# Kernel tuning notes

Measured on AMD Instinct MI355X. Metric: run time of the kernel, lower is better.

Reference implementation:

```python
import jax, jax.numpy as jnp
import numpy as np


def _conv_bn_relu(x, w, b, stride):
    # Conv2d(k=3, pad=1) with eval-mode BatchNorm folded into (w, b) at setup, then ReLU.
    y = jax.lax.conv_general_dilated(x, w, (stride, stride), ((1, 1), (1, 1)),
                                     dimension_numbers=('NCHW', 'OIHW', 'NCHW'))
    return jax.nn.relu(y + b[None, :, None, None])


def _affine_grid(theta, H, W):
    # torch.nn.functional.affine_grid, align_corners=False
    xs = (2.0 * jnp.arange(W, dtype=theta.dtype) + 1.0) / W - 1.0  # [W]
    ys = (2.0 * jnp.arange(H, dtype=theta.dtype) + 1.0) / H - 1.0  # [H]
    gx = theta[:, 0, 0, None, None] * xs[None, None, :] + theta[:, 0, 1, None, None] * ys[None, :, None] + theta[:, 0, 2, None, None]
    gy = theta[:, 1, 0, None, None] * xs[None, None, :] + theta[:, 1, 1, None, None] * ys[None, :, None] + theta[:, 1, 2, None, None]
    return jnp.stack([gx, gy], axis=-1)  # [B,H,W,2]


def _grid_sample_bilinear_zeros(im, grid):
    # torch.nn.functional.grid_sample, mode='bilinear', padding_mode='zeros', align_corners=False
    B, C, H, W = im.shape
    ix = ((grid[..., 0] + 1.0) * W - 1.0) * 0.5  # [B,H,W] pixel x coords
    iy = ((grid[..., 1] + 1.0) * H - 1.0) * 0.5
    x0 = jnp.floor(ix); y0 = jnp.floor(iy)
    x1 = x0 + 1.0;      y1 = y0 + 1.0
    wx1 = ix - x0; wx0 = 1.0 - wx1
    wy1 = iy - y0; wy0 = 1.0 - wy1
    imt = jnp.transpose(im, (0, 2, 3, 1))  # BHWC for channel-last gather
    bidx = jnp.arange(B)[:, None, None]

    def gather(xf, yf):
        valid = ((xf >= 0) & (xf <= W - 1) & (yf >= 0) & (yf <= H - 1)).astype(im.dtype)
        xi = jnp.clip(xf.astype(jnp.int32), 0, W - 1)
        yi = jnp.clip(yf.astype(jnp.int32), 0, H - 1)
        return imt[bidx, yi, xi] * valid[..., None]  # [B,H,W,C]

    out = (gather(x0, y0) * (wx0 * wy0)[..., None]
           + gather(x1, y0) * (wx1 * wy0)[..., None]
           + gather(x0, y1) * (wx0 * wy1)[..., None]
           + gather(x1, y1) * (wx1 * wy1)[..., None])
    return jnp.transpose(out, (0, 3, 1, 2))  # back to NCHW


def _forward(im_tensor, w1, b1, w2, b2, w3, b3, w4, b4, w5, b5, w6, b6,
             fw1, fb1, fw2, fb2, fw3, fb3):
    B, _, H, W = im_tensor.shape
    x1 = _conv_bn_relu(im_tensor, w1, b1, 1)
    x2 = _conv_bn_relu(jnp.concatenate([x1, im_tensor], 1), w2, b2, 2)
    x3 = _conv_bn_relu(x2, w3, b3, 1)
    x4 = _conv_bn_relu(jnp.concatenate([x3, x2], 1), w4, b4, 2)
    x5 = _conv_bn_relu(x4, w5, b5, 1)
    xs = _conv_bn_relu(jnp.concatenate([x5, x4], 1), w6, b6, 2)
    xs = xs.reshape(B, -1)  # [B, 24*(H/8)*(W/8)]
    h = jax.nn.relu(xs @ fw1.T + fb1)
    h = jax.nn.relu(h @ fw2.T + fb2)
    sz = h @ fw3.T + fb3  # [B, 4]
    # mode == 'normal': vectorized theta construction (original loops over batch)
    theta = jnp.zeros((B, 2, 3), dtype=im_tensor.dtype)
    theta = theta.at[:, 0, 0].set(jax.nn.sigmoid(sz[:, 0]))
    theta = theta.at[:, 0, 2].set(jnp.tanh(sz[:, 2]))
    theta = theta.at[:, 1, 1].set(jax.nn.sigmoid(sz[:, 1]))
    theta = theta.at[:, 1, 2].set(jnp.tanh(sz[:, 3]))
    grid = _affine_grid(theta, H, W)
    im_cropped = _grid_sample_bilinear_zeros(im_tensor, grid)
    return im_cropped, theta


def setup_inputs() -> dict:
    key = jax.random.key(0)
    B, H, W = 32, 256, 256
    keys = iter(jax.random.split(key, 64))
    nk = lambda: next(keys)
    im = jax.random.normal(nk(), (B, 1, H, W), jnp.float32)

    def conv_params(cin, cout):
        w = jax.random.normal(nk(), (cout, cin, 3, 3), jnp.float32) * (1.0 / np.sqrt(cin * 9))
        b = jax.random.normal(nk(), (cout,), jnp.float32) * 0.01
        # eval-mode BatchNorm params, folded into conv weight/bias (exact same math)
        gamma = 1.0 + 0.1 * jax.random.normal(nk(), (cout,), jnp.float32)
        beta = 0.1 * jax.random.normal(nk(), (cout,), jnp.float32)
        mean = 0.1 * jax.random.normal(nk(), (cout,), jnp.float32)
        var = jnp.abs(1.0 + 0.1 * jax.random.normal(nk(), (cout,), jnp.float32))
        scale = gamma / jnp.sqrt(var + 1e-5)
        return w * scale[:, None, None, None], b * scale + (beta - mean * scale)

    w1, b1 = conv_params(1, 8)
    w2, b2 = conv_params(9, 8)
    w3, b3 = conv_params(8, 16)
    w4, b4 = conv_params(24, 16)
    w5, b5 = conv_params(16, 24)
    w6, b6 = conv_params(40, 24)
    feat = 24 * (H // 8) * (W // 8)
    fw1 = jax.random.normal(nk(), (1024, feat), jnp.float32) * (1.0 / np.sqrt(feat))
    fb1 = jnp.zeros((1024,), jnp.float32)
    fw2 = jax.random.normal(nk(), (32, 1024), jnp.float32) * (1.0 / np.sqrt(1024))
    fb2 = jnp.zeros((32,), jnp.float32)
    fw3 = jax.random.normal(nk(), (4, 32), jnp.float32) * 0.01  # small perturbation of zero-init
    fb3 = jnp.array([1.0, 1.0, 0.0, 0.0], jnp.float32)
    return dict(im_tensor=im, w1=w1, b1=b1, w2=w2, b2=b2, w3=w3, b3=b3,
                w4=w4, b4=b4, w5=w5, b5=b5, w6=w6, b6=b6,
                fw1=fw1, fb1=fb1, fw2=fw2, fb2=fb2, fw3=fw3, fb3=fb3)


def reference(im_tensor, w1, b1, w2, b2, w3, b3, w4, b4, w5, b5, w6, b6,
              fw1, fb1, fw2, fb2, fw3, fb3):
    return _forward(im_tensor, w1, b1, w2, b2, w3, b3, w4, b4, w5, b5, w6, b6,
                    fw1, fb1, fw2, fb2, fw3, fb3)
```

## Files before the change

kernel.cpp:

```cpp
#include <hip/hip_runtime.h>
#include <hip/hip_bf16.h>

template <int CIN1, int CIN2, int COUT, int CG, int CCH, int MINW>
__global__ __launch_bounds__(256, MINW) void convq_k(
    const float* __restrict__ in1, const float* __restrict__ in2,
    const float* __restrict__ w,
    const float* __restrict__ bias,
    float* __restrict__ out,
    int Hin, int Win)
{
    constexpr int CIN = CIN1 + CIN2;
    constexpr int NG  = COUT / CG;
    constexpr int NCH = CIN / CCH;
    constexpr int P   = 34;
    constexpr int NF4 = 10;
    constexpr int WL  = NF4 * 4;
    constexpr int E4  = CCH * P * NF4;
    constexpr int NLD = (E4 + 255) / 256;
    __shared__ __align__(16) float Xs[2][CCH][P][WL];

    const int Ho = Hin, Wo = Win;
    const int tpr = Wo / 32, tpc = Ho / 32;
    int bid = blockIdx.x;
    const int tx = bid % tpr; bid /= tpr;
    const int ty = bid % tpc; bid /= tpc;
    const int g  = bid % NG;  bid /= NG;
    const int b  = bid;
    const int cbase = g * CG;

    const int tid = threadIdx.x;
    const int lx = tid & 15, ly = tid >> 4;

    const int y0 = ty * 32 - 1;
    const int xA = tx * 32 - 4;
    const int HW = Hin * Win;

    float acc[CG][4];
#pragma unroll
    for (int co = 0; co < CG; ++co) {
        float bv = bias[cbase + co];
#pragma unroll
        for (int p = 0; p < 4; ++p) acc[co][p] = bv;
    }

    int cA[NLD], lOff[NLD], em[NLD];
    bool eok[NLD], rowk[NLD], f4[NLD];
    const float* b1p[NLD];
    const float* b2p[NLD];
#pragma unroll
    for (int l = 0; l < NLD; ++l) {
        int e = tid + l * 256;
        eok[l] = (e < E4);
        int ee = eok[l] ? e : 0;
        int c  = ee / (P * NF4), r = ee % (P * NF4);
        int py = r / NF4,        jx = r % NF4;
        cA[l]   = c;
        lOff[l] = ee;
        int gy = y0 + py, c0 = xA + jx * 4;
        rowk[l] = eok[l] && ((unsigned)gy < (unsigned)Hin);
        f4[l]   = (c0 >= 0) && (c0 + 4 <= Win);
        em[l] = 0;
#pragma unroll
        for (int e2 = 0; e2 < 4; ++e2)
            if ((unsigned)(c0 + e2) < (unsigned)Win) em[l] |= 1 << e2;
        b1p[l] = (const float*)((const char*)in1 +
                 ((ptrdiff_t)(b * CIN1 + c) * HW + (ptrdiff_t)gy * Win + c0)
                 * (ptrdiff_t)sizeof(float));
        b2p[l] = (CIN2 > 0)
            ? (const float*)((const char*)in2 +
                 ((ptrdiff_t)(b * CIN2 + c - CIN1) * HW + (ptrdiff_t)gy * Win + c0)
                 * (ptrdiff_t)sizeof(float))
            : b1p[l];
    }

    float4 stg[NLD];

    auto issue = [&](int cc) {
        const size_t adv = (size_t)cc * HW;
#pragma unroll
        for (int l = 0; l < NLD; ++l) {
            float4 v = {0.0f, 0.0f, 0.0f, 0.0f};
            if (rowk[l]) {
                int ci = cc + cA[l];
                const float* p = (CIN2 == 0 || ci < CIN1) ? (b1p[l] + adv)
                                                          : (b2p[l] + adv);
                if (f4[l]) {
                    v = *(const float4*)p;
                } else {
                    float* vp = reinterpret_cast<float*>(&v);
#pragma unroll
                    for (int e2 = 0; e2 < 4; ++e2)
                        if (em[l] & (1 << e2)) vp[e2] = p[e2];
                }
            }
            stg[l] = v;
        }
    };
    auto commit = [&](int bf) {
        float4* dst = (float4*)&Xs[0][0][0][0] + (size_t)bf * (CCH * P * NF4);
#pragma unroll
        for (int l = 0; l < NLD; ++l)
            if (eok[l]) dst[lOff[l]] = stg[l];
    };

    issue(0);
    commit(0);
    __syncthreads();

    const int cb = 2 * lx + 3;

    int buf = 0;
    for (int ch = 0; ch < NCH; ++ch) {
        if (ch + 1 < NCH) issue((ch + 1) * CCH);
#pragma unroll
        for (int c = 0; c < CCH; ++c) {
#pragma unroll
            for (int ky = 0; ky < 3; ++ky) {
                const float* x0 = &Xs[buf][c][2 * ly + ky][cb];
                const float* x1 = &Xs[buf][c][2 * ly + ky + 1][cb];
                float a0 = x0[0], a1 = x0[1], a2 = x0[2], a3 = x0[3];
                float b0 = x1[0], b1v = x1[1], b2v = x1[2], b3 = x1[3];
#pragma unroll
                for (int co = 0; co < CG; ++co) {
                    const float* wp = w +
                        ((size_t)(cbase + co) * CIN + ch * CCH + c) * 9 + ky * 3;
                    float w0 = wp[0], w1 = wp[1], w2 = wp[2];
                    acc[co][0] = fmaf(a0, w0, acc[co][0]);
                    acc[co][0] = fmaf(a1, w1, acc[co][0]);
                    acc[co][0] = fmaf(a2, w2, acc[co][0]);
                    acc[co][1] = fmaf(a1, w0, acc[co][1]);
                    acc[co][1] = fmaf(a2, w1, acc[co][1]);
                    acc[co][1] = fmaf(a3, w2, acc[co][1]);
                    acc[co][2] = fmaf(b0, w0, acc[co][2]);
                    acc[co][2] = fmaf(b1v, w1, acc[co][2]);
                    acc[co][2] = fmaf(b2v, w2, acc[co][2]);
                    acc[co][3] = fmaf(b1v, w0, acc[co][3]);
                    acc[co][3] = fmaf(b2v, w1, acc[co][3]);
                    acc[co][3] = fmaf(b3, w2, acc[co][3]);
                }
            }
        }
        if (ch + 1 < NCH) {
            commit(buf ^ 1);
            __syncthreads();
            buf ^= 1;
        }
    }

    const int oy = ty * 32 + 2 * ly;
    const int ox = tx * 32 + 2 * lx;
#pragma unroll
    for (int co = 0; co < CG; ++co)
#pragma unroll
        for (int dy = 0; dy < 2; ++dy) {
            float2 v;
            v.x = fmaxf(acc[co][dy * 2 + 0], 0.0f);
            v.y = fmaxf(acc[co][dy * 2 + 1], 0.0f);
            *(float2*)&out[((size_t)(b * COUT + cbase + co) * Ho + oy + dy) * Wo + ox] = v;
        }
}

template <int CIN1, int CIN2, int COUT, int CG, int STRIDE, int CCH, int MINW>
__global__ __launch_bounds__(256, MINW) void conv2p_k(
    const float* __restrict__ in1, const float* __restrict__ in2,
    const float* __restrict__ w,
    const float* __restrict__ bias,
    float* __restrict__ out,
    int Hin, int Win)
{
    constexpr int CIN = CIN1 + CIN2;
    constexpr int NG  = COUT / CG;
    constexpr int NCH = CIN / CCH;
    constexpr int P   = 16 * STRIDE + 2;
    constexpr int NF4 = (STRIDE == 1) ? 10 : 17;
    constexpr int WL  = NF4 * 4;
    constexpr int E4  = CCH * P * NF4;
    constexpr int NLD = (E4 + 255) / 256;
    __shared__ __align__(16) float Xs[2][CCH][P][WL];

    const int Ho = Hin / STRIDE, Wo = Win / STRIDE;
    const int tpr = Wo / 32, tpc = Ho / 16;
    int bid = blockIdx.x;
    const int tx = bid % tpr; bid /= tpr;
    const int ty = bid % tpc; bid /= tpc;
    const int g  = bid % NG;  bid /= NG;
    const int b  = bid;
    const int cbase = g * CG;

    const int tid = threadIdx.x;
    const int lx = tid & 15, ly = tid >> 4;

    const int y0 = ty * 16 * STRIDE - 1;
    const int xA = tx * 32 * STRIDE - 4;
    const int HW = Hin * Win;

    float2 acc[CG];
#pragma unroll
    for (int co = 0; co < CG; ++co) {
        float bv = bias[cbase + co];
        acc[co].x = bv; acc[co].y = bv;
    }

    int cA[NLD], lOff[NLD], em[NLD];
    bool eok[NLD], rowk[NLD], f4[NLD];
    const float* b1p[NLD];
    const float* b2p[NLD];
#pragma unroll
    for (int l = 0; l < NLD; ++l) {
        int e = tid + l * 256;
        eok[l] = (e < E4);
        int ee = eok[l] ? e : 0;
        int c  = ee / (P * NF4), r = ee % (P * NF4);
        int py = r / NF4,        jx = r % NF4;
        cA[l]   = c;
        lOff[l] = ee;
        int gy = y0 + py, c0 = xA + jx * 4;
        rowk[l] = eok[l] && ((unsigned)gy < (unsigned)Hin);
        f4[l]   = (c0 >= 0) && (c0 + 4 <= Win);
        em[l] = 0;
#pragma unroll
        for (int e2 = 0; e2 < 4; ++e2)
            if ((unsigned)(c0 + e2) < (unsigned)Win) em[l] |= 1 << e2;
        b1p[l] = (const float*)((const char*)in1 +
                 ((ptrdiff_t)(b * CIN1 + c) * HW + (ptrdiff_t)gy * Win + c0)
                 * (ptrdiff_t)sizeof(float));
        b2p[l] = (CIN2 > 0)
            ? (const float*)((const char*)in2 +
                 ((ptrdiff_t)(b * CIN2 + c - CIN1) * HW + (ptrdiff_t)gy * Win + c0)
                 * (ptrdiff_t)sizeof(float))
            : b1p[l];
    }

    float4 stg[NLD];

    auto issue = [&](int cc) {
        const size_t adv = (size_t)cc * HW;
#pragma unroll
        for (int l = 0; l < NLD; ++l) {
            float4 v = {0.0f, 0.0f, 0.0f, 0.0f};
            if (rowk[l]) {
                int ci = cc + cA[l];
                const float* p = (CIN2 == 0 || ci < CIN1) ? (b1p[l] + adv)
                                                          : (b2p[l] + adv);
                if (f4[l]) {
                    v = *(const float4*)p;
                } else {
                    float* vp = reinterpret_cast<float*>(&v);
#pragma unroll
                    for (int e2 = 0; e2 < 4; ++e2)
                        if (em[l] & (1 << e2)) vp[e2] = p[e2];
                }
            }
            stg[l] = v;
        }
    };
    auto commit = [&](int bf) {
        float4* dst = (float4*)&Xs[0][0][0][0] + (size_t)bf * (CCH * P * NF4);
#pragma unroll
        for (int l = 0; l < NLD; ++l)
            if (eok[l]) dst[lOff[l]] = stg[l];
    };

    issue(0);
    commit(0);
    __syncthreads();

    const int cb = (2 * lx) * STRIDE + 3;

    int buf = 0;
    for (int ch = 0; ch < NCH; ++ch) {
        if (ch + 1 < NCH) issue((ch + 1) * CCH);
#pragma unroll
        for (int c = 0; c < CCH; ++c) {
#pragma unroll
            for (int ky = 0; ky < 3; ++ky) {
                const float* xr = &Xs[buf][c][ly * STRIDE + ky][0];
                float2 r0, r1, r2;
                r0.x = xr[cb + 0]; r0.y = xr[cb + 0 + STRIDE];
                r1.x = xr[cb + 1]; r1.y = xr[cb + 1 + STRIDE];
                r2.x = xr[cb + 2]; r2.y = xr[cb + 2 + STRIDE];
#pragma unroll
                for (int co = 0; co < CG; ++co) {
                    const float* wp = w +
                        ((size_t)(cbase + co) * CIN + ch * CCH + c) * 9 + ky * 3;
                    float w0 = wp[0], w1 = wp[1], w2 = wp[2];
                    float2 a = acc[co];
                    a.x = fmaf(r0.x, w0, a.x); a.y = fmaf(r0.y, w0, a.y);
                    a.x = fmaf(r1.x, w1, a.x); a.y = fmaf(r1.y, w1, a.y);
                    a.x = fmaf(r2.x, w2, a.x); a.y = fmaf(r2.y, w2, a.y);
                    acc[co] = a;
                }
            }
        }
        if (ch + 1 < NCH) {
            commit(buf ^ 1);
            __syncthreads();
            buf ^= 1;
        }
    }

    const int oy = ty * 16 + ly;
    const int ox = tx * 32 + 2 * lx;
#pragma unroll
    for (int co = 0; co < CG; ++co) {
        float2 v;
        v.x = fmaxf(acc[co].x, 0.0f);
        v.y = fmaxf(acc[co].y, 0.0f);
        *(float2*)&out[((size_t)(b * COUT + cbase + co) * Ho + oy) * Wo + ox] = v;
    }
}

#define FC1_K 24576
#define FC1_N 1024
#define FC1_M 32
#define FC1_KS 32
#define FC1_KC 768
#define FC1_KP 64
#define FC1_NT 64

__global__ __launch_bounds__(256) void fc1_stage_k(
    const float* __restrict__ xs,
    const float* __restrict__ fw1,
    float* __restrict__ part)
{
    __shared__ __align__(16) float As[FC1_KP][36];
    __shared__ __align__(16) float Bs[FC1_KP][66];

    const int tid = threadIdx.x;
    const int n0 = blockIdx.x * FC1_NT;
    const int ks = blockIdx.y;
    const int k0 = ks * FC1_KC;
    const int lane = tid & 63;
    const int grp = tid >> 6;

    const int m4 = (tid & 7) * 4;
    const int n2 = (tid >> 3) * 2;

    float acc[4][2];
#pragma unroll
    for (int i = 0; i < 4; ++i)
#pragma unroll
        for (int j = 0; j < 2; ++j) acc[i][j] = 0.0f;

    for (int p = 0; p < FC1_KC / FC1_KP; ++p) {
        const int kc = k0 + p * FC1_KP;
#pragma unroll
        for (int r = 0; r < 8; ++r) {
            int m = grp * 8 + r;
            As[lane][m] = xs[(size_t)m * FC1_K + kc + lane];
        }
#pragma unroll
        for (int r = 0; r < 16; ++r) {
            int nl = grp * 16 + r;
            Bs[lane][nl] = fw1[(size_t)(n0 + nl) * FC1_K + kc + lane];
        }
        __syncthreads();
#pragma unroll 8
        for (int k = 0; k < FC1_KP; ++k) {
            float4 a = *(const float4*)&As[k][m4];
            float2 bv = *(const float2*)&Bs[k][n2];
            acc[0][0] += a.x * bv.x; acc[0][1] += a.x * bv.y;
            acc[1][0] += a.y * bv.x; acc[1][1] += a.y * bv.y;
            acc[2][0] += a.z * bv.x; acc[2][1] += a.z * bv.y;
            acc[3][0] += a.w * bv.x; acc[3][1] += a.w * bv.y;
        }
        __syncthreads();
    }
#pragma unroll
    for (int i = 0; i < 4; ++i)
#pragma unroll
        for (int j = 0; j < 2; ++j)
            part[((size_t)ks * FC1_M + (m4 + i)) * FC1_N + n0 + n2 + j] = acc[i][j];
}

__global__ __launch_bounds__(256) void fc1_reduce_k(
    const float* __restrict__ part, const float* __restrict__ fb1,
    float* __restrict__ h1)
{
    int idx = blockIdx.x * 256 + threadIdx.x;
    int n = idx & (FC1_N - 1);
    int m = idx >> 10;
    float s = fb1[n];
#pragma unroll
    for (int ks = 0; ks < FC1_KS; ++ks)
        s += part[((size_t)ks * FC1_M + m) * FC1_N + n];
    h1[idx] = fmaxf(s, 0.0f);
}

__global__ __launch_bounds__(256) void fc2_k(
    const float* __restrict__ h1, const float* __restrict__ fw2,
    const float* __restrict__ fb2, float* __restrict__ h2)
{
    __shared__ float hs[1024];
    const int m = blockIdx.x;
    const int tid = threadIdx.x;
    for (int i = tid; i < 1024; i += 256) hs[i] = h1[m * 1024 + i];
    __syncthreads();
    const int wave = tid >> 6, lane = tid & 63;
#pragma unroll 1
    for (int nn = 0; nn < 8; ++nn) {
        int n = wave * 8 + nn;
        float p = 0.0f;
        for (int k = lane; k < 1024; k += 64)
            p += fw2[n * 1024 + k] * hs[k];
#pragma unroll
        for (int off = 32; off; off >>= 1) p += __shfl_xor(p, off);
        if (lane == 0) h2[m * 32 + n] = fmaxf(p + fb2[n], 0.0f);
    }
}

__global__ void fc3_theta_k(
    const float* __restrict__ h2, const float* __restrict__ fw3,
    const float* __restrict__ fb3, float* __restrict__ theta_out)
{
    int t = threadIdx.x;
    if (t >= 128) return;
    int m = t >> 2, j = t & 3;
    float s = fb3[j];
#pragma unroll
    for (int k = 0; k < 32; ++k) s += h2[m * 32 + k] * fw3[j * 32 + k];
    float* th = theta_out + m * 6;
    if (j == 0)      { th[0] = 1.0f / (1.0f + expf(-s)); th[1] = 0.0f; }
    else if (j == 1) { th[4] = 1.0f / (1.0f + expf(-s)); th[3] = 0.0f; }
    else if (j == 2) { th[2] = tanhf(s); }
    else             { th[5] = tanhf(s); }
}

__global__ __launch_bounds__(256) void sampler_k(
    const float* __restrict__ im, const float* __restrict__ theta,
    float* __restrict__ out)
{
    int idx = blockIdx.x * 256 + threadIdx.x;
    int x = idx & 255;
    int y = (idx >> 8) & 255;
    int b = idx >> 16;
    const float* th = theta + b * 6;
    float xsn = (2.0f * x + 1.0f) * (1.0f / 256.0f) - 1.0f;
    float ysn = (2.0f * y + 1.0f) * (1.0f / 256.0f) - 1.0f;
    float gx = th[0] * xsn + th[1] * ysn + th[2];
    float gy = th[3] * xsn + th[4] * ysn + th[5];
    float ix = ((gx + 1.0f) * 256.0f - 1.0f) * 0.5f;
    float iy = ((gy + 1.0f) * 256.0f - 1.0f) * 0.5f;
    float x0 = floorf(ix), y0 = floorf(iy);
    float wx1 = ix - x0, wy1 = iy - y0;
    float wx0 = 1.0f - wx1, wy0 = 1.0f - wy1;
    const float* src = im + (size_t)b * 65536;

    auto g = [&](float xf, float yf) -> float {
        if (xf < 0.0f || xf > 255.0f || yf < 0.0f || yf > 255.0f) return 0.0f;
        int xi = (int)xf, yi = (int)yf;
        return src[yi * 256 + xi];
    };
    float v00 = g(x0, y0);
    float v10 = g(x0 + 1.0f, y0);
    float v01 = g(x0, y0 + 1.0f);
    float v11 = g(x0 + 1.0f, y0 + 1.0f);
    out[idx] = v00 * wx0 * wy0 + v10 * wx1 * wy0 + v01 * wx0 * wy1 + v11 * wx1 * wy1;
}

extern "C" void kernel_launch(void* const* d_in, const int* in_sizes, int n_in,
                              void* d_out, int out_size, void* d_ws, size_t ws_size,
                              hipStream_t stream)
{
    const float* im  = (const float*)d_in[0];
    const float* w1  = (const float*)d_in[1];  const float* b1 = (const float*)d_in[2];
    const float* w2  = (const float*)d_in[3];  const float* b2 = (const float*)d_in[4];
    const float* w3  = (const float*)d_in[5];  const float* b3 = (const float*)d_in[6];
    const float* w4  = (const float*)d_in[7];  const float* b4 = (const float*)d_in[8];
    const float* w5  = (const float*)d_in[9];  const float* b5 = (const float*)d_in[10];
    const float* w6  = (const float*)d_in[11]; const float* b6 = (const float*)d_in[12];
    const float* fw1 = (const float*)d_in[13]; const float* fb1 = (const float*)d_in[14];
    const float* fw2 = (const float*)d_in[15]; const float* fb2 = (const float*)d_in[16];
    const float* fw3 = (const float*)d_in[17]; const float* fb3 = (const float*)d_in[18];

    float* out = (float*)d_out;
    float* ws  = (float*)d_ws;

    float* x2   = ws + 0;
    float* x1c  = ws + 4194304;
    float* x3   = ws + 4194304;
    float* x4   = ws + 12582912;
    float* x5   = ws + 4194304;
    float* x6   = ws + 14680064;
    float* part = ws + 0;
    float* h1   = ws + 1048576;
    float* h2   = ws + 1081344;

    float* theta = out + 32 * 65536;

    for (int c = 0; c < 2; ++c) {
        const float* imc = im + (size_t)c * 16 * 65536;
        convq_k<1, 0, 8, 8, 1, 4><<<16 * 1 * 8 * 8, 256, 0, stream>>>(
            imc, nullptr, w1, b1, x1c, 256, 256);
        conv2p_k<8, 1, 8, 8, 2, 1, 6><<<16 * 8 * 4, 256, 0, stream>>>(
            x1c, imc, w2, b2, x2 + (size_t)c * 2097152, 256, 256);
    }
    convq_k<8, 0, 16, 8, 2, 4><<<32 * 2 * 4 * 4, 256, 0, stream>>>(
        x2, nullptr, w3, b3, x3, 128, 128);
    conv2p_k<16, 8, 16, 8, 2, 1, 6><<<32 * 2 * 2 * 4, 256, 0, stream>>>(
        x3, x2, w4, b4, x4, 128, 128);
    convq_k<16, 0, 24, 6, 2, 4><<<32 * 4 * 2 * 2, 256, 0, stream>>>(
        x4, nullptr, w5, b5, x5, 64, 64);
    conv2p_k<24, 16, 24, 4, 2, 1, 6><<<32 * 2 * 1 * 6, 256, 0, stream>>>(
        x5, x4, w6, b6, x6, 64, 64);

    fc1_stage_k<<<dim3(16, FC1_KS), 256, 0, stream>>>(x6, fw1, part);
    fc1_reduce_k<<<128, 256, 0, stream>>>(part, fb1, h1);
    fc2_k<<<32, 256, 0, stream>>>(h1, fw2, fb2, h2);
    fc3_theta_k<<<1, 128, 0, stream>>>(h2, fw3, fb3, theta);

    sampler_k<<<8192, 256, 0, stream>>>(im, theta, out);
}
```

Baseline: 283.3 us.

## Fuse FC tail kernels, vectorize fc1 weight loads, batch first convs when workspace allows

```diff
diff --git a/kernel.cpp b/kernel.cpp
--- a/kernel.cpp
+++ b/kernel.cpp
@@ -336,6 +336,9 @@
     const int m4 = (tid & 7) * 4;
     const int n2 = (tid >> 3) * 2;
 
+    const int bk4 = (tid & 15) * 4;
+    const int bnl = tid >> 4;
+
     float acc[4][2];
 #pragma unroll
     for (int i = 0; i < 4; ++i)
@@ -350,9 +353,13 @@
             As[lane][m] = xs[(size_t)m * FC1_K + kc + lane];
         }
 #pragma unroll
-        for (int r = 0; r < 16; ++r) {
-            int nl = grp * 16 + r;
-            Bs[lane][nl] = fw1[(size_t)(n0 + nl) * FC1_K + kc + lane];
+        for (int r = 0; r < 4; ++r) {
+            int nl = r * 16 + bnl;
+            float4 v = *(const float4*)&fw1[(size_t)(n0 + nl) * FC1_K + kc + bk4];
+            Bs[bk4 + 0][nl] = v.x;
+            Bs[bk4 + 1][nl] = v.y;
+            Bs[bk4 + 2][nl] = v.z;
+            Bs[bk4 + 3][nl] = v.w;
         }
         __syncthreads();
 #pragma unroll 8
@@ -373,29 +380,26 @@
             part[((size_t)ks * FC1_M + (m4 + i)) * FC1_N + n0 + n2 + j] = acc[i][j];
 }
 
-__global__ __launch_bounds__(256) void fc1_reduce_k(
+__global__ __launch_bounds__(256) void fc_tail_k(
     const float* __restrict__ part, const float* __restrict__ fb1,
-    float* __restrict__ h1)
-{
-    int idx = blockIdx.x * 256 + threadIdx.x;
-    int n = idx & (FC1_N - 1);
-    int m = idx >> 10;
-    float s = fb1[n];
-#pragma unroll
-    for (int ks = 0; ks < FC1_KS; ++ks)
-        s += part[((size_t)ks * FC1_M + m) * FC1_N + n];
-    h1[idx] = fmaxf(s, 0.0f);
-}
-
-__global__ __launch_bounds__(256) void fc2_k(
-    const float* __restrict__ h1, const float* __restrict__ fw2,
-    const float* __restrict__ fb2, float* __restrict__ h2)
+    const float* __restrict__ fw2,  const float* __restrict__ fb2,
+    const float* __restrict__ fw3,  const float* __restrict__ fb3,
+    float* __restrict__ theta_out)
 {
     __shared__ float hs[1024];
+    __shared__ float h2s[32];
     const int m = blockIdx.x;
     const int tid = threadIdx.x;
-    for (int i = tid; i < 1024; i += 256) hs[i] = h1[m * 1024 + i];
+
+    for (int n = tid; n < FC1_N; n += 256) {
+        float s = fb1[n];
+#pragma unroll
+        for (int ks = 0; ks < FC1_KS; ++ks)
+            s += part[((size_t)ks * FC1_M + m) * FC1_N + n];
+        hs[n] = fmaxf(s, 0.0f);
+    }
     __syncthreads();
+
     const int wave = tid >> 6, lane = tid & 63;
 #pragma unroll 1
     for (int nn = 0; nn < 8; ++nn) {
@@ -405,25 +409,21 @@
             p += fw2[n * 1024 + k] * hs[k];
 #pragma unroll
         for (int off = 32; off; off >>= 1) p += __shfl_xor(p, off);
-        if (lane == 0) h2[m * 32 + n] = fmaxf(p + fb2[n], 0.0f);
-    }
-}
-
-__global__ void fc3_theta_k(
-    const float* __restrict__ h2, const float* __restrict__ fw3,
-    const float* __restrict__ fb3, float* __restrict__ theta_out)
-{
-    int t = threadIdx.x;
-    if (t >= 128) return;
-    int m = t >> 2, j = t & 3;
-    float s = fb3[j];
-#pragma unroll
-    for (int k = 0; k < 32; ++k) s += h2[m * 32 + k] * fw3[j * 32 + k];
-    float* th = theta_out + m * 6;
-    if (j == 0)      { th[0] = 1.0f / (1.0f + expf(-s)); th[1] = 0.0f; }
-    else if (j == 1) { th[4] = 1.0f / (1.0f + expf(-s)); th[3] = 0.0f; }
-    else if (j == 2) { th[2] = tanhf(s); }
-    else             { th[5] = tanhf(s); }
+        if (lane == 0) h2s[n] = fmaxf(p + fb2[n], 0.0f);
+    }
+    __syncthreads();
+
+    if (tid < 4) {
+        int j = tid;
+        float s = fb3[j];
+#pragma unroll
+        for (int k = 0; k < 32; ++k) s += h2s[k] * fw3[j * 32 + k];
+        float* th = theta_out + m * 6;
+        if (j == 0)      { th[0] = 1.0f / (1.0f + expf(-s)); th[1] = 0.0f; }
+        else if (j == 1) { th[4] = 1.0f / (1.0f + expf(-s)); th[3] = 0.0f; }
+        else if (j == 2) { th[2] = tanhf(s); }
+        else             { th[5] = tanhf(s); }
+    }
 }
 
 __global__ __launch_bounds__(256) void sampler_k(
@@ -476,38 +476,61 @@
     float* out = (float*)d_out;
     float* ws  = (float*)d_ws;
 
+    float* theta = out + 32 * 65536;
+
+    const bool big = ws_size >= (size_t)20971520 * 4;
+
     float* x2   = ws + 0;
-    float* x1c  = ws + 4194304;
-    float* x3   = ws + 4194304;
-    float* x4   = ws + 12582912;
-    float* x5   = ws + 4194304;
-    float* x6   = ws + 14680064;
     float* part = ws + 0;
-    float* h1   = ws + 1048576;
-    float* h2   = ws + 1081344;
-
-    float* theta = out + 32 * 65536;
-
-    for (int c = 0; c < 2; ++c) {
-        const float* imc = im + (size_t)c * 16 * 65536;
-        convq_k<1, 0, 8, 8, 1, 4><<<16 * 1 * 8 * 8, 256, 0, stream>>>(
-            imc, nullptr, w1, b1, x1c, 256, 256);
-        conv2p_k<8, 1, 8, 8, 2, 1, 6><<<16 * 8 * 4, 256, 0, stream>>>(
-            x1c, imc, w2, b2, x2 + (size_t)c * 2097152, 256, 256);
-    }
-    convq_k<8, 0, 16, 8, 2, 4><<<32 * 2 * 4 * 4, 256, 0, stream>>>(
-        x2, nullptr, w3, b3, x3, 128, 128);
-    conv2p_k<16, 8, 16, 8, 2, 1, 6><<<32 * 2 * 2 * 4, 256, 0, stream>>>(
-        x3, x2, w4, b4, x4, 128, 128);
-    convq_k<16, 0, 24, 6, 2, 4><<<32 * 4 * 2 * 2, 256, 0, stream>>>(
-        x4, nullptr, w5, b5, x5, 64, 64);
-    conv2p_k<24, 16, 24, 4, 2, 1, 6><<<32 * 2 * 1 * 6, 256, 0, stream>>>(
-        x5, x4, w6, b6, x6, 64, 64);
-
-    fc1_stage_k<<<dim3(16, FC1_KS), 256, 0, stream>>>(x6, fw1, part);
-    fc1_reduce_k<<<128, 256, 0, stream>>>(part, fb1, h1);
-    fc2_k<<<32, 256, 0, stream>>>(h1, fw2, fb2, h2);
-    fc3_theta_k<<<1, 128, 0, stream>>>(h2, fw3, fb3, theta);
+
+    if (big) {
+        float* x1 = ws + 4194304;
+        float* x3 = ws + 4194304;
+        float* x4 = ws + 12582912;
+        float* x5 = ws + 14680064;
+        float* x6 = ws + 17825792;
+
+        convq_k<1, 0, 8, 8, 1, 4><<<2048, 256, 0, stream>>>(
+            im, nullptr, w1, b1, x1, 256, 256);
+        conv2p_k<8, 1, 8, 8, 2, 1, 6><<<1024, 256, 0, stream>>>(
+            x1, im, w2, b2, x2, 256, 256);
+        convq_k<8, 0, 16, 8, 2, 4><<<1024, 256, 0, stream>>>(
+            x2, nullptr, w3, b3, x3, 128, 128);
+        conv2p_k<16, 8, 16, 8, 2, 1, 6><<<512, 256, 0, stream>>>(
+            x3, x2, w4, b4, x4, 128, 128);
+        convq_k<16, 0, 24, 6, 2, 4><<<512, 256, 0, stream>>>(
+            x4, nullptr, w5, b5, x5, 64, 64);
+        conv2p_k<24, 16, 24, 4, 2, 1, 6><<<384, 256, 0, stream>>>(
+            x5, x4, w6, b6, x6, 64, 64);
+
+        fc1_stage_k<<<dim3(16, FC1_KS), 256, 0, stream>>>(x6, fw1, part);
+        fc_tail_k<<<32, 256, 0, stream>>>(part, fb1, fw2, fb2, fw3, fb3, theta);
+    } else {
+        float* x1c = ws + 4194304;
+        float* x3  = ws + 4194304;
+        float* x4  = ws + 12582912;
+        float* x5  = ws + 4194304;
+        float* x6  = ws + 14680064;
+
+        for (int c = 0; c < 2; ++c) {
+            const float* imc = im + (size_t)c * 16 * 65536;
+            convq_k<1, 0, 8, 8, 1, 4><<<1024, 256, 0, stream>>>(
+                imc, nullptr, w1, b1, x1c, 256, 256);
+            conv2p_k<8, 1, 8, 8, 2, 1, 6><<<512, 256, 0, stream>>>(
+                x1c, imc, w2, b2, x2 + (size_t)c * 2097152, 256, 256);
+        }
+        convq_k<8, 0, 16, 8, 2, 4><<<1024, 256, 0, stream>>>(
+            x2, nullptr, w3, b3, x3, 128, 128);
+        conv2p_k<16, 8, 16, 8, 2, 1, 6><<<512, 256, 0, stream>>>(
+            x3, x2, w4, b4, x4, 128, 128);
+        convq_k<16, 0, 24, 6, 2, 4><<<512, 256, 0, stream>>>(
+            x4, nullptr, w5, b5, x5, 64, 64);
+        conv2p_k<24, 16, 24, 4, 2, 1, 6><<<384, 256, 0, stream>>>(
+            x5, x4, w6, b6, x6, 64, 64);
+
+        fc1_stage_k<<<dim3(16, FC1_KS), 256, 0, stream>>>(x6, fw1, part);
+        fc_tail_k<<<32, 256, 0, stream>>>(part, fb1, fw2, fb2, fw3, fb3, theta);
+    }
 
     sampler_k<<<8192, 256, 0, stream>>>(im, theta, out);
 }
```

After: 267.5 us, median of 2. -5.6%, faster.
